# Kernel tuning notes

Hardware: AMD Instinct MI355X
Metric: run time of the kernel (lower is better)

The kernel has to match this reference:

```python
import jax, jax.numpy as jnp
import numpy as np
import math

B, S, I, HD, T, N = 4096, 96, 64, 128, 24, 64  # batch, enc seq, input_dim, hidden, output_dim, temp_node


def setup_inputs() -> dict:
    key = jax.random.key(0)
    ks = jax.random.split(key, 13)
    stdv = 1.0 / math.sqrt(HD)
    return {
        "H": jax.random.normal(ks[0], (B, S, I), jnp.float32),
        "y0": jax.random.normal(ks[1], (B, 1), jnp.float32),
        "h0": jax.random.normal(ks[2], (B, HD), jnp.float32) * stdv,
        "c0": jax.random.normal(ks[3], (B, HD), jnp.float32) * stdv,
        "Wa": jax.random.normal(ks[4], (I, T, N), jnp.float32) * stdv,
        "Ua": jax.random.normal(ks[5], (HD, T, N), jnp.float32) * stdv,
        "ba": jax.random.normal(ks[6], (T, N), jnp.float32) * stdv,
        "Va": jax.random.normal(ks[7], (N, T, 1), jnp.float32) * stdv,
        "W": jax.random.normal(ks[8], (I + 1, 4 * HD), jnp.float32) * stdv,
        "U": jax.random.normal(ks[9], (HD, 4 * HD), jnp.float32) * stdv,
        "bias": jax.random.normal(ks[10], (4 * HD,), jnp.float32) * stdv,
        "fc_w": jax.random.normal(ks[11], (T, HD), jnp.float32) * stdv,
        "fc_b": jax.random.normal(ks[12], (T,), jnp.float32) * stdv,
    }


def reference(H, y0, h0, c0, Wa, Ua, ba, Va, W, U, bias, fc_w, fc_b):
    hd = h0.shape[1]
    scale = 1.0 / jnp.sqrt(jnp.asarray(hd, H.dtype))
    # stack per-step params with step axis leading for lax.scan
    Wa_s = jnp.transpose(Wa, (1, 0, 2))      # [T, I, N]
    Ua_s = jnp.transpose(Ua, (1, 0, 2))      # [T, HD, N]
    Va_s = jnp.transpose(Va[:, :, 0], (1, 0))  # [T, N]

    def step(carry, xs):
        h_st, c_st, y_prev = carry
        wa, ua, ba_t, va, fw, fb = xs
        # temporal attention over encoder positions, queried by LSTM cell state
        score = jnp.tanh(jnp.einsum('bsi,in->bsn', H, wa)
                         + (c_st @ ua)[:, None, :] + ba_t)      # [B,S,N]
        beta = jax.nn.softmax(jnp.einsum('bsn,n->bs', score, va) * scale, axis=1)  # [B,S]
        ctx = jnp.einsum('bs,bsi->bi', beta, H)                 # [B,I]
        x = jnp.concatenate([ctx, y_prev], axis=1)              # [B,I+1]
        gates = x @ W + h_st @ U + bias                         # [B,4HD]
        i_g, f_g, g_g, o_g = jnp.split(gates, 4, axis=1)
        c_new = jax.nn.sigmoid(f_g) * c_st + jax.nn.sigmoid(i_g) * jnp.tanh(g_g)
        h_new = jax.nn.sigmoid(o_g) * jnp.tanh(c_new)
        y_t = h_new @ fw[:, None] + fb                          # [B,1]
        return (h_new, c_new, y_t), (h_new, y_t[:, 0])

    _, (hs, ys) = jax.lax.scan(step, (h0, c0, y0),
                               (Wa_s, Ua_s, ba, Va_s, fc_w, fc_b))
    y_seq = jnp.transpose(ys, (1, 0))           # [B, T]
    hidden_seq = jnp.transpose(hs, (1, 0, 2))   # [B, T, HD]
    return y_seq, hidden_seq
```

## Files before the change

### kernel.cpp

```cpp
#include <hip/hip_runtime.h>
#include <hip/hip_bf16.h>

#define B 4096
#define S 96
#define I_DIM 64
#define HD 128
#define T_STEPS 24
#define N_DIM 64
#define G4 512
#define BPB 16

typedef unsigned short u16;
typedef __attribute__((ext_vector_type(8))) short bf16x8;
typedef __attribute__((ext_vector_type(4))) float f32x4;

__device__ __forceinline__ u16 f2b(float f) {
    unsigned int u = __float_as_uint(f);
    unsigned int r = (u + 0x7FFFu + ((u >> 16) & 1u)) >> 16;
    return (u16)r;
}
__device__ __forceinline__ float b2f(u16 x) {
    return __uint_as_float(((unsigned int)x) << 16);
}
__device__ __forceinline__ float frcp(float x) { return __builtin_amdgcn_rcpf(x); }
__device__ __forceinline__ float sigm_f(float x) { return frcp(1.0f + __expf(-x)); }
__device__ __forceinline__ float tanh_f(float x) {
    x = fminf(fmaxf(x, -15.f), 15.f);
    float e = __expf(2.0f * x);
    return 1.0f - 2.0f * frcp(e + 1.0f);
}


__global__ __launch_bounds__(256)
void k_init(const float* __restrict__ h0, const float* __restrict__ c0,
            const float* __restrict__ y0,
            float* __restrict__ h_ws, float* __restrict__ c_ws,
            float* __restrict__ y_ws)
{
    int idx = blockIdx.x * 256 + threadIdx.x;
    if (idx < B * HD) {
        h_ws[idx] = h0[idx];
        c_ws[idx] = c0[idx];
    }
    if (idx < B) y_ws[idx] = y0[idx];
}

__global__ __launch_bounds__(256)
void k_prep(const float* __restrict__ H, u16* __restrict__ Hb)
{
    size_t idx = (size_t)blockIdx.x * 256 + threadIdx.x;
    const float4* src = reinterpret_cast<const float4*>(H) + idx * 2;
    float4 v0 = src[0], v1 = src[1];
    ushort4 p0 = { f2b(v0.x), f2b(v0.y), f2b(v0.z), f2b(v0.w) };
    ushort4 p1 = { f2b(v1.x), f2b(v1.y), f2b(v1.z), f2b(v1.w) };
    ushort4* dst = reinterpret_cast<ushort4*>(Hb + idx * 8);
    dst[0] = p0;
    dst[1] = p1;
}

__global__ __launch_bounds__(64)
void k_prep_S(const float* __restrict__ Wa, u16* __restrict__ BfragS)
{
    int bi = blockIdx.x;
    int t = bi >> 3, nt = (bi >> 1) & 3, ks = bi & 1;
    int l = threadIdx.x;
    int n = nt * 16 + (l & 15);
    u16 outv[8];
    #pragma unroll
    for (int j = 0; j < 8; ++j) {
        int i = ks * 32 + ((l >> 4) * 8) + j;
        outv[j] = f2b(Wa[(size_t)i * (T_STEPS * N_DIM) + t * N_DIM + n]);
    }
    *reinterpret_cast<int4*>(BfragS + ((size_t)(bi * 64 + l)) * 8) =
        *reinterpret_cast<const int4*>(outv);
}

__global__ __launch_bounds__(64)
void k_prep_G(const float* __restrict__ W, const float* __restrict__ U,
              u16* __restrict__ GH, u16* __restrict__ GL)
{
    int bi = blockIdx.x;
    int ks = bi >> 5, nt = bi & 31;
    int l = threadIdx.x;
    int col = nt * 16 + (l & 15);
    u16 hv[8], lv[8];
    #pragma unroll
    for (int j = 0; j < 8; ++j) {
        int k = ks * 32 + ((l >> 4) * 8) + j;
        float v = (k < 64) ? W[(size_t)k * G4 + col] : U[(size_t)(k - 64) * G4 + col];
        unsigned int ub = __float_as_uint(v);
        u16 hi = (u16)(ub >> 16);
        hv[j] = hi;
        lv[j] = f2b(v - b2f(hi));
    }
    size_t base = ((size_t)(bi * 64 + l)) * 8;
    *reinterpret_cast<int4*>(GH + base) = *reinterpret_cast<const int4*>(hv);
    *reinterpret_cast<int4*>(GL + base) = *reinterpret_cast<const int4*>(lv);
}

__global__ __launch_bounds__(256)
void k_prep_U(const float* __restrict__ Ua, float* __restrict__ UaT)
{
    int idx = blockIdx.x * 256 + threadIdx.x;
    int hd = idx & 127, n = (idx >> 7) & 63, t = idx >> 13;
    UaT[(size_t)t * 8192 + n * 128 + hd] = Ua[(size_t)hd * (T_STEPS * N_DIM) + t * N_DIM + n];
}

__global__ __launch_bounds__(256)
void k_prep_V(const float* __restrict__ Va, float* __restrict__ VaT)
{
    int idx = blockIdx.x * 256 + threadIdx.x;
    int n = idx & 63, t = idx >> 6;
    VaT[t * 64 + n] = Va[n * T_STEPS + t];
}

template<bool PRE>
__global__ __launch_bounds__(1024)
void k_step(const float* __restrict__ H, const u16* __restrict__ Hb,
            const u16* __restrict__ BfragS, const u16* __restrict__ GH,
            const u16* __restrict__ GL, const float* __restrict__ UaT,
            const float* __restrict__ VaT, const float* __restrict__ ba,
            const float* __restrict__ W, const float* __restrict__ bias,
            const float* __restrict__ fc_w, const float* __restrict__ fc_b,
            float* __restrict__ y_ws, float* __restrict__ h_ws,
            float* __restrict__ c_ws, float* __restrict__ out, int t)
{
    __shared__ float cs[BPB][HD];
    __shared__ float hsv[BPB][HD];
    __shared__ float lg[BPB][S];
    __shared__ float xs[BPB][I_DIM];
    __shared__ float yv[BPB];
    __shared__ float gates[BPB][G4];
    __shared__ __align__(16) u16 AFh[6][BPB][32];
    __shared__ __align__(16) u16 AFl[6][BPB][32];
    __shared__ float UaL[N_DIM][HD + 1];

    const int tid = threadIdx.x;
    const int w = tid >> 6, l = tid & 63;
    const int b0 = blockIdx.x * BPB, b = b0 + w;

    {
        const float4* src = reinterpret_cast<const float4*>(UaT + (size_t)t * 8192);
        #pragma unroll
        for (int k = 0; k < 2; ++k) {
            int e4 = tid + 1024 * k;
            float4 v = src[e4];
            int e = e4 * 4;
            int n = e >> 7, hd = e & 127;
            UaL[n][hd]     = v.x;
            UaL[n][hd + 1] = v.y;
            UaL[n][hd + 2] = v.z;
            UaL[n][hd + 3] = v.w;
        }
    }
    {
        cs[w][l]        = c_ws[(size_t)b * HD + l];
        cs[w][l + 64]   = c_ws[(size_t)b * HD + l + 64];
        hsv[w][l]       = h_ws[(size_t)b * HD + l];
        hsv[w][l + 64]  = h_ws[(size_t)b * HD + l + 64];
    }
    if (tid < BPB) yv[tid] = y_ws[b0 + tid];
    __syncthreads();

    bf16x8 bfr[4][2];
    {
        const bf16x8* bsp = reinterpret_cast<const bf16x8*>(BfragS) + (size_t)t * 8 * 64 + l;
        #pragma unroll
        for (int nt = 0; nt < 4; ++nt)
            #pragma unroll
            for (int ks = 0; ks < 2; ++ks)
                bfr[nt][ks] = bsp[(nt * 2 + ks) * 64];
    }

    float cbn;
    {
        float p = 0.0f;
        #pragma unroll 16
        for (int hd = 0; hd < HD; ++hd)
            p += UaL[l][hd] * cs[w][hd];
        cbn = p + ba[t * 64 + l];
    }
    float van = VaT[t * 64 + l];
    float cbv[4], vav[4];
    #pragma unroll
    for (int nt = 0; nt < 4; ++nt) {
        int n = nt * 16 + (l & 15);
        cbv[nt] = __shfl(cbn, n, 64);
        vav[nt] = __shfl(van, n, 64);
    }

    const float scale = 0.08838834764831845f;
    const u16* hbase = Hb + (size_t)b * (S * I_DIM);
    const float* hbasef = H + (size_t)b * (S * I_DIM);
    const int kp = (l >> 4) * 8;
    for (int mt = 0; mt < 6; ++mt) {
        int row = mt * 16 + (l & 15);
        bf16x8 a0, a1;
        if (PRE) {
            a0 = *reinterpret_cast<const bf16x8*>(hbase + row * I_DIM + kp);
            a1 = *reinterpret_cast<const bf16x8*>(hbase + row * I_DIM + 32 + kp);
        } else {
            const float* hr = hbasef + row * I_DIM;
            u16 t0[8], t1[8];
            #pragma unroll
            for (int j = 0; j < 8; ++j) {
                t0[j] = f2b(hr[kp + j]);
                t1[j] = f2b(hr[32 + kp + j]);
            }
            a0 = *reinterpret_cast<const bf16x8*>(t0);
            a1 = *reinterpret_cast<const bf16x8*>(t1);
        }
        float lgp[4] = {0.f, 0.f, 0.f, 0.f};
        #pragma unroll
        for (int nt = 0; nt < 4; ++nt) {
            f32x4 c = {0.f, 0.f, 0.f, 0.f};
            c = __builtin_amdgcn_mfma_f32_16x16x32_bf16(a0, bfr[nt][0], c, 0, 0, 0);
            c = __builtin_amdgcn_mfma_f32_16x16x32_bf16(a1, bfr[nt][1], c, 0, 0, 0);
            #pragma unroll
            for (int i = 0; i < 4; ++i) {
                float sc = c[i] + cbv[nt];
                sc = fminf(fmaxf(sc, -15.f), 15.f);
                float e = __expf(2.0f * sc);
                float th = 1.0f - 2.0f * frcp(e + 1.0f);
                lgp[i] += th * vav[nt];
            }
        }
        #pragma unroll
        for (int off = 1; off < 16; off <<= 1)
            #pragma unroll
            for (int i = 0; i < 4; ++i) lgp[i] += __shfl_xor(lgp[i], off, 64);
        if ((l & 15) == 0) {
            int g = l >> 4;
            #pragma unroll
            for (int i = 0; i < 4; ++i)
                lg[w][mt * 16 + g * 4 + i] = lgp[i] * scale;
        }
    }

    {
        float v0 = lg[w][l];
        float v1 = (l < 32) ? lg[w][64 + l] : -1e30f;
        float m = fmaxf(v0, v1);
        #pragma unroll
        for (int off = 32; off; off >>= 1) m = fmaxf(m, __shfl_xor(m, off, 64));
        float e0 = __expf(v0 - m);
        float e1 = (l < 32) ? __expf(v1 - m) : 0.0f;
        float ss = e0 + e1;
        #pragma unroll
        for (int off = 32; off; off >>= 1) ss += __shfl_xor(ss, off, 64);
        float inv = frcp(ss);
        lg[w][l] = e0 * inv;
        if (l < 32) lg[w][64 + l] = e1 * inv;
    }

    {
        float ctxp[8] = {0.f, 0.f, 0.f, 0.f, 0.f, 0.f, 0.f, 0.f};
        #pragma unroll
        for (int k = 0; k < 12; ++k) {
            int chunk = l + 64 * k;
            int s = chunk >> 3;
            float beta = lg[w][s];
            if (PRE) {
                int4 v = reinterpret_cast<const int4*>(hbase)[chunk];
                const u16* pv = reinterpret_cast<const u16*>(&v);
                #pragma unroll
                for (int j = 0; j < 8; ++j) ctxp[j] += beta * b2f(pv[j]);
            } else {
                const float4* pf = reinterpret_cast<const float4*>(hbasef) + chunk * 2;
                float4 v0 = pf[0], v1 = pf[1];
                ctxp[0] += beta * v0.x; ctxp[1] += beta * v0.y;
                ctxp[2] += beta * v0.z; ctxp[3] += beta * v0.w;
                ctxp[4] += beta * v1.x; ctxp[5] += beta * v1.y;
                ctxp[6] += beta * v1.z; ctxp[7] += beta * v1.w;
            }
        }
        #pragma unroll
        for (int off = 8; off <= 32; off <<= 1)
            #pragma unroll
            for (int j = 0; j < 8; ++j) ctxp[j] += __shfl_xor(ctxp[j], off, 64);
        if (l < 8) {
            #pragma unroll
            for (int j = 0; j < 8; ++j) xs[w][l * 8 + j] = ctxp[j];
        }
    }
    __syncthreads();

    #pragma unroll
    for (int it = 0; it < 3; ++it) {
        int idx = tid + 1024 * it;
        int ks = idx >> 9, rem = idx & 511;
        int r = rem >> 5, kk = rem & 31;
        int k = ks * 32 + kk;
        float f = (k < 64) ? xs[r][k] : hsv[r][k - 64];
        unsigned int ub = __float_as_uint(f);
        u16 hi = (u16)(ub >> 16);
        AFh[ks][r][kk] = hi;
        AFl[ks][r][kk] = f2b(f - b2f(hi));
    }
    __syncthreads();

    {
        f32x4 acc[2] = {{0.f,0.f,0.f,0.f},{0.f,0.f,0.f,0.f}};
        const int nt0 = w * 2;
        const int r = l & 15;
        #pragma unroll
        for (int ks = 0; ks < 6; ++ks) {
            bf16x8 ah = *reinterpret_cast<const bf16x8*>(&AFh[ks][r][kp]);
            bf16x8 al = *reinterpret_cast<const bf16x8*>(&AFl[ks][r][kp]);
            #pragma unroll
            for (int c2 = 0; c2 < 2; ++c2) {
                size_t base = ((size_t)(ks * 32 + nt0 + c2) * 64 + l);
                bf16x8 bh = reinterpret_cast<const bf16x8*>(GH)[base];
                bf16x8 bl = reinterpret_cast<const bf16x8*>(GL)[base];
                acc[c2] = __builtin_amdgcn_mfma_f32_16x16x32_bf16(ah, bh, acc[c2], 0, 0, 0);
                acc[c2] = __builtin_amdgcn_mfma_f32_16x16x32_bf16(ah, bl, acc[c2], 0, 0, 0);
                acc[c2] = __builtin_amdgcn_mfma_f32_16x16x32_bf16(al, bh, acc[c2], 0, 0, 0);
            }
        }
        {
            int i0 = (l >> 4) * 4;
            #pragma unroll
            for (int c2 = 0; c2 < 2; ++c2) {
                int j = (nt0 + c2) * 16 + (l & 15);
                float bj = bias[j];
                float wy = W[(size_t)I_DIM * G4 + j];
                #pragma unroll
                for (int i = 0; i < 4; ++i)
                    gates[i0 + i][j] = acc[c2][i] + bj + yv[i0 + i] * wy;
            }
        }
    }
    __syncthreads();

    {
        float yp = 0.0f;
        #pragma unroll
        for (int m = 0; m < 2; ++m) {
            int hd = l + 64 * m;
            float ig = gates[w][hd];
            float fg = gates[w][HD + hd];
            float gg = gates[w][2 * HD + hd];
            float og = gates[w][3 * HD + hd];
            float cold = cs[w][hd];
            float cnew = sigm_f(fg) * cold + sigm_f(ig) * tanh_f(gg);
            float hnew = sigm_f(og) * tanh_f(cnew);
            c_ws[(size_t)b * HD + hd] = cnew;
            h_ws[(size_t)b * HD + hd] = hnew;
            out[(size_t)(B * T_STEPS) + ((size_t)b * T_STEPS + t) * HD + hd] = hnew;
            yp += hnew * fc_w[t * HD + hd];
        }
        #pragma unroll
        for (int off = 32; off; off >>= 1) yp += __shfl_xor(yp, off, 64);
        if (l == 0) {
            float y = yp + fc_b[t];
            y_ws[b] = y;
            out[(size_t)b * T_STEPS + t] = y;
        }
    }
}

extern "C" void kernel_launch(void* const* d_in, const int* in_sizes, int n_in,
                              void* d_out, int out_size, void* d_ws, size_t ws_size,
                              hipStream_t stream)
{
    const float* H    = (const float*)d_in[0];
    const float* y0   = (const float*)d_in[1];
    const float* h0   = (const float*)d_in[2];
    const float* c0   = (const float*)d_in[3];
    const float* Wa   = (const float*)d_in[4];
    const float* Ua   = (const float*)d_in[5];
    const float* ba   = (const float*)d_in[6];
    const float* Va   = (const float*)d_in[7];
    const float* W    = (const float*)d_in[8];
    const float* U    = (const float*)d_in[9];
    const float* bias = (const float*)d_in[10];
    const float* fc_w = (const float*)d_in[11];
    const float* fc_b = (const float*)d_in[12];
    float* out = (float*)d_out;

    u16* BfragS = (u16*)d_ws;
    u16* GH     = BfragS + 98304;
    u16* GL     = GH + 98304;
    float* UaT  = (float*)(GL + 98304);
    float* VaT  = UaT + 196608;
    float* h_ws = VaT + 1536;
    float* c_ws = h_ws + (size_t)B * HD;
    float* y_ws = c_ws + (size_t)B * HD;
    u16*   Hb   = (u16*)(y_ws + B);

    size_t need = (size_t)((char*)(Hb + (size_t)B * S * I_DIM) - (char*)d_ws);
    bool pre = ws_size >= need;

    k_init<<<dim3((B * HD + 255) / 256), dim3(256), 0, stream>>>(h0, c0, y0, h_ws, c_ws, y_ws);
    k_prep_S<<<dim3(192), dim3(64), 0, stream>>>(Wa, BfragS);
    k_prep_G<<<dim3(192), dim3(64), 0, stream>>>(W, U, GH, GL);
    k_prep_U<<<dim3(768), dim3(256), 0, stream>>>(Ua, UaT);
    k_prep_V<<<dim3(6), dim3(256), 0, stream>>>(Va, VaT);
    if (pre)
        k_prep<<<dim3(B * S * I_DIM / 8 / 256), dim3(256), 0, stream>>>(H, Hb);

    for (int t = 0; t < T_STEPS; ++t) {
        if (pre)
            k_step<true><<<dim3(B / BPB), dim3(1024), 0, stream>>>(H, Hb, BfragS, GH, GL,
                UaT, VaT, ba, W, bias, fc_w, fc_b, y_ws, h_ws, c_ws, out, t);
        else
            k_step<false><<<dim3(B / BPB), dim3(1024), 0, stream>>>(H, Hb, BfragS, GH, GL,
                UaT, VaT, ba, W, bias, fc_w, fc_b, y_ws, h_ws, c_ws, out, t);
    }
}
```

Baseline: 606.6 us.

## Fuse two recurrent timesteps per kernel launch, keeping state in shared memory

Each step kernel now runs two consecutive LSTM/attention timesteps, carrying h, c and y in shared memory between them and writing state back to global memory only at the end. This halves the number of launches and cuts the global state round-trips. It may also improve L2 reuse of the per-batch H rows across the two steps. A new barrier guards the per-step UaL reload, and the longer kernel body may raise register pressure.

```diff
diff --git a/kernel.cpp b/kernel.cpp
--- a/kernel.cpp
+++ b/kernel.cpp
@@ -116,14 +116,14 @@
 
 template<bool PRE>
 __global__ __launch_bounds__(1024)
-void k_step(const float* __restrict__ H, const u16* __restrict__ Hb,
-            const u16* __restrict__ BfragS, const u16* __restrict__ GH,
-            const u16* __restrict__ GL, const float* __restrict__ UaT,
-            const float* __restrict__ VaT, const float* __restrict__ ba,
-            const float* __restrict__ W, const float* __restrict__ bias,
-            const float* __restrict__ fc_w, const float* __restrict__ fc_b,
-            float* __restrict__ y_ws, float* __restrict__ h_ws,
-            float* __restrict__ c_ws, float* __restrict__ out, int t)
+void k_step2(const float* __restrict__ H, const u16* __restrict__ Hb,
+             const u16* __restrict__ BfragS, const u16* __restrict__ GH,
+             const u16* __restrict__ GL, const float* __restrict__ UaT,
+             const float* __restrict__ VaT, const float* __restrict__ ba,
+             const float* __restrict__ W, const float* __restrict__ bias,
+             const float* __restrict__ fc_w, const float* __restrict__ fc_b,
+             float* __restrict__ y_ws, float* __restrict__ h_ws,
+             float* __restrict__ c_ws, float* __restrict__ out, int t0)
 {
     __shared__ float cs[BPB][HD];
     __shared__ float hsv[BPB][HD];
@@ -139,20 +139,11 @@
     const int w = tid >> 6, l = tid & 63;
     const int b0 = blockIdx.x * BPB, b = b0 + w;
 
-    {
-        const float4* src = reinterpret_cast<const float4*>(UaT + (size_t)t * 8192);
-        #pragma unroll
-        for (int k = 0; k < 2; ++k) {
-            int e4 = tid + 1024 * k;
-            float4 v = src[e4];
-            int e = e4 * 4;
-            int n = e >> 7, hd = e & 127;
-            UaL[n][hd]     = v.x;
-            UaL[n][hd + 1] = v.y;
-            UaL[n][hd + 2] = v.z;
-            UaL[n][hd + 3] = v.w;
-        }
-    }
+    const u16* hbase = Hb + (size_t)b * (S * I_DIM);
+    const float* hbasef = H + (size_t)b * (S * I_DIM);
+    const int kp = (l >> 4) * 8;
+    const float scale = 0.08838834764831845f;
+
     {
         cs[w][l]        = c_ws[(size_t)b * HD + l];
         cs[w][l + 64]   = c_ws[(size_t)b * HD + l + 64];
@@ -160,203 +151,229 @@
         hsv[w][l + 64]  = h_ws[(size_t)b * HD + l + 64];
     }
     if (tid < BPB) yv[tid] = y_ws[b0 + tid];
-    __syncthreads();
-
-    bf16x8 bfr[4][2];
-    {
-        const bf16x8* bsp = reinterpret_cast<const bf16x8*>(BfragS) + (size_t)t * 8 * 64 + l;
-        #pragma unroll
-        for (int nt = 0; nt < 4; ++nt)
-            #pragma unroll
-            for (int ks = 0; ks < 2; ++ks)
-                bfr[nt][ks] = bsp[(nt * 2 + ks) * 64];
-    }
-
-    float cbn;
-    {
-        float p = 0.0f;
-        #pragma unroll 16
-        for (int hd = 0; hd < HD; ++hd)
-            p += UaL[l][hd] * cs[w][hd];
-        cbn = p + ba[t * 64 + l];
-    }
-    float van = VaT[t * 64 + l];
-    float cbv[4], vav[4];
-    #pragma unroll
-    for (int nt = 0; nt < 4; ++nt) {
-        int n = nt * 16 + (l & 15);
-        cbv[nt] = __shfl(cbn, n, 64);
-        vav[nt] = __shfl(van, n, 64);
-    }
-
-    const float scale = 0.08838834764831845f;
-    const u16* hbase = Hb + (size_t)b * (S * I_DIM);
-    const float* hbasef = H + (size_t)b * (S * I_DIM);
-    const int kp = (l >> 4) * 8;
-    for (int mt = 0; mt < 6; ++mt) {
-        int row = mt * 16 + (l & 15);
-        bf16x8 a0, a1;
-        if (PRE) {
-            a0 = *reinterpret_cast<const bf16x8*>(hbase + row * I_DIM + kp);
-            a1 = *reinterpret_cast<const bf16x8*>(hbase + row * I_DIM + 32 + kp);
-        } else {
-            const float* hr = hbasef + row * I_DIM;
-            u16 t0[8], t1[8];
-            #pragma unroll
-            for (int j = 0; j < 8; ++j) {
-                t0[j] = f2b(hr[kp + j]);
-                t1[j] = f2b(hr[32 + kp + j]);
-            }
-            a0 = *reinterpret_cast<const bf16x8*>(t0);
-            a1 = *reinterpret_cast<const bf16x8*>(t1);
-        }
-        float lgp[4] = {0.f, 0.f, 0.f, 0.f};
+
+    auto step_body = [&](int t) {
+        {
+            const float4* src = reinterpret_cast<const float4*>(UaT + (size_t)t * 8192);
+            #pragma unroll
+            for (int k = 0; k < 2; ++k) {
+                int e4 = tid + 1024 * k;
+                float4 v = src[e4];
+                int e = e4 * 4;
+                int n = e >> 7, hd = e & 127;
+                UaL[n][hd]     = v.x;
+                UaL[n][hd + 1] = v.y;
+                UaL[n][hd + 2] = v.z;
+                UaL[n][hd + 3] = v.w;
+            }
+        }
+        __syncthreads();
+
+        bf16x8 bfr[4][2];
+        {
+            const bf16x8* bsp = reinterpret_cast<const bf16x8*>(BfragS) + (size_t)t * 8 * 64 + l;
+            #pragma unroll
+            for (int nt = 0; nt < 4; ++nt)
+                #pragma unroll
+                for (int ks = 0; ks < 2; ++ks)
+                    bfr[nt][ks] = bsp[(nt * 2 + ks) * 64];
+        }
+
+        float cbn;
+        {
+            float p = 0.0f;
+            #pragma unroll 16
+            for (int hd = 0; hd < HD; ++hd)
+                p += UaL[l][hd] * cs[w][hd];
+            cbn = p + ba[t * 64 + l];
+        }
+        float van = VaT[t * 64 + l];
+        float cbv[4], vav[4];
         #pragma unroll
         for (int nt = 0; nt < 4; ++nt) {
-            f32x4 c = {0.f, 0.f, 0.f, 0.f};
-            c = __builtin_amdgcn_mfma_f32_16x16x32_bf16(a0, bfr[nt][0], c, 0, 0, 0);
-            c = __builtin_amdgcn_mfma_f32_16x16x32_bf16(a1, bfr[nt][1], c, 0, 0, 0);
-            #pragma unroll
-            for (int i = 0; i < 4; ++i) {
-                float sc = c[i] + cbv[nt];
-                sc = fminf(fmaxf(sc, -15.f), 15.f);
-                float e = __expf(2.0f * sc);
-                float th = 1.0f - 2.0f * frcp(e + 1.0f);
-                lgp[i] += th * vav[nt];
-            }
-        }
+            int n = nt * 16 + (l & 15);
+            cbv[nt] = __shfl(cbn, n, 64);
+            vav[nt] = __shfl(van, n, 64);
+        }
+
+        for (int mt = 0; mt < 6; ++mt) {
+            int row = mt * 16 + (l & 15);
+            bf16x8 a0, a1;
+            if (PRE) {
+                a0 = *reinterpret_cast<const bf16x8*>(hbase + row * I_DIM + kp);
+                a1 = *reinterpret_cast<const bf16x8*>(hbase + row * I_DIM + 32 + kp);
+            } else {
+                const float* hr = hbasef + row * I_DIM;
+                u16 t0v[8], t1v[8];
+                #pragma unroll
+                for (int j = 0; j < 8; ++j) {
+                    t0v[j] = f2b(hr[kp + j]);
+                    t1v[j] = f2b(hr[32 + kp + j]);
+                }
+                a0 = *reinterpret_cast<const bf16x8*>(t0v);
+                a1 = *reinterpret_cast<const bf16x8*>(t1v);
+            }
+            float lgp[4] = {0.f, 0.f, 0.f, 0.f};
+            #pragma unroll
+            for (int nt = 0; nt < 4; ++nt) {
+                f32x4 c = {0.f, 0.f, 0.f, 0.f};
+                c = __builtin_amdgcn_mfma_f32_16x16x32_bf16(a0, bfr[nt][0], c, 0, 0, 0);
+                c = __builtin_amdgcn_mfma_f32_16x16x32_bf16(a1, bfr[nt][1], c, 0, 0, 0);
+                #pragma unroll
+                for (int i = 0; i < 4; ++i) {
+                    float sc = c[i] + cbv[nt];
+                    sc = fminf(fmaxf(sc, -15.f), 15.f);
+                    float e = __expf(2.0f * sc);
+                    float th = 1.0f - 2.0f * frcp(e + 1.0f);
+                    lgp[i] += th * vav[nt];
+                }
+            }
+            #pragma unroll
+            for (int off = 1; off < 16; off <<= 1)
+                #pragma unroll
+                for (int i = 0; i < 4; ++i) lgp[i] += __shfl_xor(lgp[i], off, 64);
+            if ((l & 15) == 0) {
+                int g = l >> 4;
+                #pragma unroll
+                for (int i = 0; i < 4; ++i)
+                    lg[w][mt * 16 + g * 4 + i] = lgp[i] * scale;
+            }
+        }
+
+        {
+            float v0 = lg[w][l];
+            float v1 = (l < 32) ? lg[w][64 + l] : -1e30f;
+            float m = fmaxf(v0, v1);
+            #pragma unroll
+            for (int off = 32; off; off >>= 1) m = fmaxf(m, __shfl_xor(m, off, 64));
+            float e0 = __expf(v0 - m);
+            float e1 = (l < 32) ? __expf(v1 - m) : 0.0f;
+            float ss = e0 + e1;
+            #pragma unroll
+            for (int off = 32; off; off >>= 1) ss += __shfl_xor(ss, off, 64);
+            float inv = frcp(ss);
+            lg[w][l] = e0 * inv;
+            if (l < 32) lg[w][64 + l] = e1 * inv;
+        }
+
+        {
+            float ctxp[8] = {0.f, 0.f, 0.f, 0.f, 0.f, 0.f, 0.f, 0.f};
+            #pragma unroll
+            for (int k = 0; k < 12; ++k) {
+                int chunk = l + 64 * k;
+                int s = chunk >> 3;
+                float beta = lg[w][s];
+                if (PRE) {
+                    int4 v = reinterpret_cast<const int4*>(hbase)[chunk];
+                    const u16* pv = reinterpret_cast<const u16*>(&v);
+                    #pragma unroll
+                    for (int j = 0; j < 8; ++j) ctxp[j] += beta * b2f(pv[j]);
+                } else {
+                    const float4* pf = reinterpret_cast<const float4*>(hbasef) + chunk * 2;
+                    float4 v0 = pf[0], v1 = pf[1];
+                    ctxp[0] += beta * v0.x; ctxp[1] += beta * v0.y;
+                    ctxp[2] += beta * v0.z; ctxp[3] += beta * v0.w;
+                    ctxp[4] += beta * v1.x; ctxp[5] += beta * v1.y;
+                    ctxp[6] += beta * v1.z; ctxp[7] += beta * v1.w;
+                }
+            }
+            #pragma unroll
+            for (int off = 8; off <= 32; off <<= 1)
+                #pragma unroll
+                for (int j = 0; j < 8; ++j) ctxp[j] += __shfl_xor(ctxp[j], off, 64);
+            if (l < 8) {
+                #pragma unroll
+                for (int j = 0; j < 8; ++j) xs[w][l * 8 + j] = ctxp[j];
+            }
+        }
+        __syncthreads();
+
         #pragma unroll
-        for (int off = 1; off < 16; off <<= 1)
-            #pragma unroll
-            for (int i = 0; i < 4; ++i) lgp[i] += __shfl_xor(lgp[i], off, 64);
-        if ((l & 15) == 0) {
-            int g = l >> 4;
-            #pragma unroll
-            for (int i = 0; i < 4; ++i)
-                lg[w][mt * 16 + g * 4 + i] = lgp[i] * scale;
-        }
-    }
+        for (int it = 0; it < 3; ++it) {
+            int idx = tid + 1024 * it;
+            int ks = idx >> 9, rem = idx & 511;
+            int r = rem >> 5, kk = rem & 31;
+            int k = ks * 32 + kk;
+            float f = (k < 64) ? xs[r][k] : hsv[r][k - 64];
+            unsigned int ub = __float_as_uint(f);
+            u16 hi = (u16)(ub >> 16);
+            AFh[ks][r][kk] = hi;
+            AFl[ks][r][kk] = f2b(f - b2f(hi));
+        }
+        __syncthreads();
+
+        {
+            f32x4 acc[2] = {{0.f,0.f,0.f,0.f},{0.f,0.f,0.f,0.f}};
+            const int nt0 = w * 2;
+            const int r = l & 15;
+            #pragma unroll
+            for (int ks = 0; ks < 6; ++ks) {
+                bf16x8 ah = *reinterpret_cast<const bf16x8*>(&AFh[ks][r][kp]);
+                bf16x8 al = *reinterpret_cast<const bf16x8*>(&AFl[ks][r][kp]);
+                #pragma unroll
+                for (int c2 = 0; c2 < 2; ++c2) {
+                    size_t base = ((size_t)(ks * 32 + nt0 + c2) * 64 + l);
+                    bf16x8 bh = reinterpret_cast<const bf16x8*>(GH)[base];
+                    bf16x8 bl = reinterpret_cast<const bf16x8*>(GL)[base];
+                    acc[c2] = __builtin_amdgcn_mfma_f32_16x16x32_bf16(ah, bh, acc[c2], 0, 0, 0);
+                    acc[c2] = __builtin_amdgcn_mfma_f32_16x16x32_bf16(ah, bl, acc[c2], 0, 0, 0);
+                    acc[c2] = __builtin_amdgcn_mfma_f32_16x16x32_bf16(al, bh, acc[c2], 0, 0, 0);
+                }
+            }
+            {
+                int i0 = (l >> 4) * 4;
+                #pragma unroll
+                for (int c2 = 0; c2 < 2; ++c2) {
+                    int j = (nt0 + c2) * 16 + (l & 15);
+                    float bj = bias[j];
+                    float wy = W[(size_t)I_DIM * G4 + j];
+                    #pragma unroll
+                    for (int i = 0; i < 4; ++i)
+                        gates[i0 + i][j] = acc[c2][i] + bj + yv[i0 + i] * wy;
+                }
+            }
+        }
+        __syncthreads();
+
+        {
+            float yp = 0.0f;
+            #pragma unroll
+            for (int m = 0; m < 2; ++m) {
+                int hd = l + 64 * m;
+                float ig = gates[w][hd];
+                float fg = gates[w][HD + hd];
+                float gg = gates[w][2 * HD + hd];
+                float og = gates[w][3 * HD + hd];
+                float cold = cs[w][hd];
+                float cnew = sigm_f(fg) * cold + sigm_f(ig) * tanh_f(gg);
+                float hnew = sigm_f(og) * tanh_f(cnew);
+                cs[w][hd] = cnew;
+                hsv[w][hd] = hnew;
+                out[(size_t)(B * T_STEPS) + ((size_t)b * T_STEPS + t) * HD + hd] = hnew;
+                yp += hnew * fc_w[t * HD + hd];
+            }
+            #pragma unroll
+            for (int off = 32; off; off >>= 1) yp += __shfl_xor(yp, off, 64);
+            if (l == 0) {
+                float y = yp + fc_b[t];
+                yv[w] = y;
+                out[(size_t)b * T_STEPS + t] = y;
+            }
+        }
+    };
+
+    step_body(t0);
+    __builtin_amdgcn_sched_barrier(0);
+    step_body(t0 + 1);
+    __syncthreads();
 
     {
-        float v0 = lg[w][l];
-        float v1 = (l < 32) ? lg[w][64 + l] : -1e30f;
-        float m = fmaxf(v0, v1);
-        #pragma unroll
-        for (int off = 32; off; off >>= 1) m = fmaxf(m, __shfl_xor(m, off, 64));
-        float e0 = __expf(v0 - m);
-        float e1 = (l < 32) ? __expf(v1 - m) : 0.0f;
-        float ss = e0 + e1;
-        #pragma unroll
-        for (int off = 32; off; off >>= 1) ss += __shfl_xor(ss, off, 64);
-        float inv = frcp(ss);
-        lg[w][l] = e0 * inv;
-        if (l < 32) lg[w][64 + l] = e1 * inv;
-    }
-
-    {
-        float ctxp[8] = {0.f, 0.f, 0.f, 0.f, 0.f, 0.f, 0.f, 0.f};
-        #pragma unroll
-        for (int k = 0; k < 12; ++k) {
-            int chunk = l + 64 * k;
-            int s = chunk >> 3;
-            float beta = lg[w][s];
-            if (PRE) {
-                int4 v = reinterpret_cast<const int4*>(hbase)[chunk];
-                const u16* pv = reinterpret_cast<const u16*>(&v);
-                #pragma unroll
-                for (int j = 0; j < 8; ++j) ctxp[j] += beta * b2f(pv[j]);
-            } else {
-                const float4* pf = reinterpret_cast<const float4*>(hbasef) + chunk * 2;
-                float4 v0 = pf[0], v1 = pf[1];
-                ctxp[0] += beta * v0.x; ctxp[1] += beta * v0.y;
-                ctxp[2] += beta * v0.z; ctxp[3] += beta * v0.w;
-                ctxp[4] += beta * v1.x; ctxp[5] += beta * v1.y;
-                ctxp[6] += beta * v1.z; ctxp[7] += beta * v1.w;
-            }
-        }
-        #pragma unroll
-        for (int off = 8; off <= 32; off <<= 1)
-            #pragma unroll
-            for (int j = 0; j < 8; ++j) ctxp[j] += __shfl_xor(ctxp[j], off, 64);
-        if (l < 8) {
-            #pragma unroll
-            for (int j = 0; j < 8; ++j) xs[w][l * 8 + j] = ctxp[j];
-        }
-    }
-    __syncthreads();
-
-    #pragma unroll
-    for (int it = 0; it < 3; ++it) {
-        int idx = tid + 1024 * it;
-        int ks = idx >> 9, rem = idx & 511;
-        int r = rem >> 5, kk = rem & 31;
-        int k = ks * 32 + kk;
-        float f = (k < 64) ? xs[r][k] : hsv[r][k - 64];
-        unsigned int ub = __float_as_uint(f);
-        u16 hi = (u16)(ub >> 16);
-        AFh[ks][r][kk] = hi;
-        AFl[ks][r][kk] = f2b(f - b2f(hi));
-    }
-    __syncthreads();
-
-    {
-        f32x4 acc[2] = {{0.f,0.f,0.f,0.f},{0.f,0.f,0.f,0.f}};
-        const int nt0 = w * 2;
-        const int r = l & 15;
-        #pragma unroll
-        for (int ks = 0; ks < 6; ++ks) {
-            bf16x8 ah = *reinterpret_cast<const bf16x8*>(&AFh[ks][r][kp]);
-            bf16x8 al = *reinterpret_cast<const bf16x8*>(&AFl[ks][r][kp]);
-            #pragma unroll
-            for (int c2 = 0; c2 < 2; ++c2) {
-                size_t base = ((size_t)(ks * 32 + nt0 + c2) * 64 + l);
-                bf16x8 bh = reinterpret_cast<const bf16x8*>(GH)[base];
-                bf16x8 bl = reinterpret_cast<const bf16x8*>(GL)[base];
-                acc[c2] = __builtin_amdgcn_mfma_f32_16x16x32_bf16(ah, bh, acc[c2], 0, 0, 0);
-                acc[c2] = __builtin_amdgcn_mfma_f32_16x16x32_bf16(ah, bl, acc[c2], 0, 0, 0);
-                acc[c2] = __builtin_amdgcn_mfma_f32_16x16x32_bf16(al, bh, acc[c2], 0, 0, 0);
-            }
-        }
-        {
-            int i0 = (l >> 4) * 4;
-            #pragma unroll
-            for (int c2 = 0; c2 < 2; ++c2) {
-                int j = (nt0 + c2) * 16 + (l & 15);
-                float bj = bias[j];
-                float wy = W[(size_t)I_DIM * G4 + j];
-                #pragma unroll
-                for (int i = 0; i < 4; ++i)
-                    gates[i0 + i][j] = acc[c2][i] + bj + yv[i0 + i] * wy;
-            }
-        }
-    }
-    __syncthreads();
-
-    {
-        float yp = 0.0f;
-        #pragma unroll
-        for (int m = 0; m < 2; ++m) {
-            int hd = l + 64 * m;
-            float ig = gates[w][hd];
-            float fg = gates[w][HD + hd];
-            float gg = gates[w][2 * HD + hd];
-            float og = gates[w][3 * HD + hd];
-            float cold = cs[w][hd];
-            float cnew = sigm_f(fg) * cold + sigm_f(ig) * tanh_f(gg);
-            float hnew = sigm_f(og) * tanh_f(cnew);
-            c_ws[(size_t)b * HD + hd] = cnew;
-            h_ws[(size_t)b * HD + hd] = hnew;
-            out[(size_t)(B * T_STEPS) + ((size_t)b * T_STEPS + t) * HD + hd] = hnew;
-            yp += hnew * fc_w[t * HD + hd];
-        }
-        #pragma unroll
-        for (int off = 32; off; off >>= 1) yp += __shfl_xor(yp, off, 64);
-        if (l == 0) {
-            float y = yp + fc_b[t];
-            y_ws[b] = y;
-            out[(size_t)b * T_STEPS + t] = y;
-        }
-    }
+        c_ws[(size_t)b * HD + l]       = cs[w][l];
+        c_ws[(size_t)b * HD + l + 64]  = cs[w][l + 64];
+        h_ws[(size_t)b * HD + l]       = hsv[w][l];
+        h_ws[(size_t)b * HD + l + 64]  = hsv[w][l + 64];
+    }
+    if (tid < BPB) y_ws[b0 + tid] = yv[tid];
 }
 
 extern "C" void kernel_launch(void* const* d_in, const int* in_sizes, int n_in,
@@ -399,12 +416,12 @@
     if (pre)
         k_prep<<<dim3(B * S * I_DIM / 8 / 256), dim3(256), 0, stream>>>(H, Hb);
 
-    for (int t = 0; t < T_STEPS; ++t) {
+    for (int t0 = 0; t0 < T_STEPS; t0 += 2) {
         if (pre)
-            k_step<true><<<dim3(B / BPB), dim3(1024), 0, stream>>>(H, Hb, BfragS, GH, GL,
-                UaT, VaT, ba, W, bias, fc_w, fc_b, y_ws, h_ws, c_ws, out, t);
+            k_step2<true><<<dim3(B / BPB), dim3(1024), 0, stream>>>(H, Hb, BfragS, GH, GL,
+                UaT, VaT, ba, W, bias, fc_w, fc_b, y_ws, h_ws, c_ws, out, t0);
         else
-            k_step<false><<<dim3(B / BPB), dim3(1024), 0, stream>>>(H, Hb, BfragS, GH, GL,
-                UaT, VaT, ba, W, bias, fc_w, fc_b, y_ws, h_ws, c_ws, out, t);
-    }
-}
+            k_step2<false><<<dim3(B / BPB), dim3(1024), 0, stream>>>(H, Hb, BfragS, GH, GL,
+                UaT, VaT, ba, W, bias, fc_w, fc_b, y_ws, h_ws, c_ws, out, t0);
+    }
+}
```

After: 937.9 us. 54.6% more time.
